# Optimization experiments

Hardware: AMD Instinct MI355X
Metric: run time of the kernel (lower is better)

The kernel has to match this reference:

```python
import jax, jax.numpy as jnp
import numpy as np

N = 50000
E = 800000
C_IN = 64
C_OUT = 64
K = 3  # Chebyshev order (num_stacks)
LAMBDA_MAX = 2.0


def setup_inputs() -> dict:
    key = jax.random.key(0)
    ks = jax.random.split(key, 32)
    inp = {
        'X': jax.random.normal(ks[0], (N, C_IN), dtype=jnp.float32),
        'edge_index': jax.random.randint(ks[1], (2, E), 0, N, dtype=jnp.int64),
        'edge_weight': jax.random.uniform(ks[2], (E,), dtype=jnp.float32),
        'H': jax.random.normal(ks[3], (N, C_OUT), dtype=jnp.float32),
        'C': jax.random.normal(ks[4], (N, C_OUT), dtype=jnp.float32),
    }
    # 8 ChebConvs: conv_{x,h}_{i,f,c,o}; x-convs map C_IN->C_OUT, h-convs C_OUT->C_OUT
    names_x = ['Wxi', 'Wxf', 'Wxc', 'Wxo']
    names_h = ['Whi', 'Whf', 'Whc', 'Who']
    i = 5
    for nx, nh in zip(names_x, names_h):
        inp[nx] = jax.random.normal(ks[i], (K, C_IN, C_OUT), dtype=jnp.float32) * (1.0 / np.sqrt(K * C_IN)); i += 1
        inp['b' + nx[1:]] = jax.random.normal(ks[i], (C_OUT,), dtype=jnp.float32) * 0.01; i += 1
        inp[nh] = jax.random.normal(ks[i], (K, C_OUT, C_OUT), dtype=jnp.float32) * (1.0 / np.sqrt(K * C_OUT)); i += 1
        inp['b' + nh[1:]] = jax.random.normal(ks[i], (C_OUT,), dtype=jnp.float32) * 0.01; i += 1
    # per-gate biases b_i, b_f, b_c, b_o of shape [1, C_OUT] (zero-initialized in torch)
    for nm in ['bi', 'bf', 'bc', 'bo']:
        inp[nm] = jax.random.normal(ks[i], (1, C_OUT), dtype=jnp.float32) * 0.01; i += 1
    return inp


def _cheb_norm(edge_index, edge_weight, n):
    # symmetric normalization: D^-1/2 W D^-1/2 (PyG get_laplacian 'sym')
    row, col = edge_index[0], edge_index[1]
    deg = jax.ops.segment_sum(edge_weight, row, num_segments=n)
    dinv = jnp.where(deg > 0, jax.lax.rsqrt(jnp.where(deg > 0, deg, 1.0)), 0.0)
    return dinv[row] * edge_weight * dinv[col]


def _cheb_conv(x, W, b, row, col, nw, n):
    # ChebConv: out = sum_k T_k(L_hat) x @ W[k] + b, with
    # L_hat v = (2/lambda_max) * (v - A_norm v) - v
    def Lhat(v):
        agg = jax.ops.segment_sum(nw[:, None] * v[col], row, num_segments=n)
        return (2.0 / LAMBDA_MAX) * (v - agg) - v
    Tx_prev = x
    out = x @ W[0]
    k = W.shape[0]
    if k > 1:
        Tx = Lhat(x)
        out = out + Tx @ W[1]
        for j in range(2, k):
            Tx_new = 2.0 * Lhat(Tx) - Tx_prev
            out = out + Tx_new @ W[j]
            Tx_prev, Tx = Tx, Tx_new
    return out + b


def reference(X, edge_index, edge_weight, H, C,
              Wxi, bxi, Whi, bhi, Wxf, bxf, Whf, bhf,
              Wxc, bxc, Whc, bhc, Wxo, bxo, Who, bho,
              bi, bf, bc, bo):
    n = X.shape[0]
    row, col = edge_index[0], edge_index[1]
    nw = _cheb_norm(edge_index, edge_weight, n)
    cc = lambda v, W, b: _cheb_conv(v, W, b, row, col, nw, n)
    I = jax.nn.sigmoid(cc(X, Wxi, bxi) + cc(H, Whi, bhi) + bi)
    F = jax.nn.sigmoid(cc(X, Wxf, bxf) + cc(H, Whf, bhf) + bf)
    T = jnp.tanh(cc(X, Wxc, bxc) + cc(H, Whc, bhc) + bc)
    C_new = F * C + I * T
    O = jax.nn.sigmoid(cc(X, Wxo, bxo) + cc(H, Who, bho) + bo)
    H_new = O * jnp.tanh(C_new)
    return (H_new, C_new)
```

## Files before the change

kernel.cpp:

```cpp
#include <hip/hip_runtime.h>

#define N_NODES 50000
#define N_PAD   50048
#define N_EDGES 800000
#define NBE4    782
#define NB_IL2  1563
#define NBKT    196
#define BCAP    4992

typedef __attribute__((ext_vector_type(8))) short bf16x8;
typedef __attribute__((ext_vector_type(4))) float f32x4;

__device__ __forceinline__ unsigned short f2bf(float f) {
    unsigned u = __float_as_uint(f);
    u = (u + 0x7fffu + ((u >> 16) & 1u)) >> 16;
    return (unsigned short)u;
}

__device__ __forceinline__ float fsig(float x) {
    x = fminf(fmaxf(x, -30.f), 30.f);
    float t = __expf(x);
    return __fdividef(t, 1.f + t);
}
__device__ __forceinline__ float ftanh(float x) {
    x = fminf(fmaxf(x, -15.f), 15.f);
    float t = __expf(2.f * x);
    return 1.f - __fdividef(2.f, t + 1.f);
}


__global__ __launch_bounds__(256) void k_prep(
    const void* __restrict__ eiraw,
    unsigned* __restrict__ hist,
    const float* __restrict__ X, const float* __restrict__ H, unsigned short* __restrict__ XH,
    const float* __restrict__ Wxi, const float* __restrict__ Whi,
    const float* __restrict__ Wxf, const float* __restrict__ Whf,
    const float* __restrict__ Wxc, const float* __restrict__ Whc,
    const float* __restrict__ Wxo, const float* __restrict__ Who,
    const float* __restrict__ bxi, const float* __restrict__ bhi,
    const float* __restrict__ bxf, const float* __restrict__ bhf,
    const float* __restrict__ bxc, const float* __restrict__ bhc,
    const float* __restrict__ bxo, const float* __restrict__ bho,
    const float* __restrict__ bgi, const float* __restrict__ bgf,
    const float* __restrict__ bgc, const float* __restrict__ bgo,
    unsigned short* __restrict__ Wf, float* __restrict__ ball) {
    __shared__ int sflag;
    __shared__ unsigned cnt[NBKT];
    int b = blockIdx.x, t = threadIdx.x;
    if (b < NBE4) {
        if (t == 0) sflag = 0;
        if (t < NBKT) cnt[t] = 0;
        __syncthreads();
        int si = b * 1024 + t;
        int sv = ((const int*)eiraw)[1 + 2 * si];
        if (sv) atomicOr(&sflag, 1);
        __syncthreads();
        int is32 = sflag;
#pragma unroll
        for (int k = 0; k < 4; k++) {
            int e = b * 1024 + k * 256 + t;
            if (e < N_EDGES) {
                int r = is32 ? ((const int*)eiraw)[e] : (int)(((const long long*)eiraw)[e]);
                atomicAdd(&cnt[r >> 8], 1u);
            }
        }
        __syncthreads();
        if (t < NBKT) hist[(size_t)t * NBE4 + b] = cnt[t];
        return;
    }
    int bb = b - NBE4;
    if (bb < NB_IL2) {
        int tt = bb * 256 + t;
        int node = tt >> 3, g = tt & 7;
        if (node >= N_NODES) return;
        const float* base = (g < 4) ? (X + (size_t)node * 64 + g * 16)
                                    : (H + (size_t)node * 64 + (g - 4) * 16);
        float4 v0 = ((const float4*)base)[0];
        float4 v1 = ((const float4*)base)[1];
        float4 v2 = ((const float4*)base)[2];
        float4 v3 = ((const float4*)base)[3];
        uint4 o0, o1;
        o0.x = (unsigned)f2bf(v0.x) | ((unsigned)f2bf(v0.y) << 16);
        o0.y = (unsigned)f2bf(v0.z) | ((unsigned)f2bf(v0.w) << 16);
        o0.z = (unsigned)f2bf(v1.x) | ((unsigned)f2bf(v1.y) << 16);
        o0.w = (unsigned)f2bf(v1.z) | ((unsigned)f2bf(v1.w) << 16);
        o1.x = (unsigned)f2bf(v2.x) | ((unsigned)f2bf(v2.y) << 16);
        o1.y = (unsigned)f2bf(v2.z) | ((unsigned)f2bf(v2.w) << 16);
        o1.z = (unsigned)f2bf(v3.x) | ((unsigned)f2bf(v3.y) << 16);
        o1.w = (unsigned)f2bf(v3.z) | ((unsigned)f2bf(v3.w) << 16);
        unsigned short* dst = XH + (size_t)node * 128 + g * 16;
        *(uint4*)dst = o0;
        *(uint4*)(dst + 8) = o1;
        return;
    }
    bb -= NB_IL2;
    if (bb < 48) {
        int flat = bb * 256 + t;
        int l = flat & 63, nt = (flat >> 6) & 15, ks = flat >> 10;
        int n = nt * 16 + (l & 15);
        int g = n >> 6, c = n & 63;
        const float* WX = (g == 0) ? Wxi : (g == 1) ? Wxf : (g == 2) ? Wxc : Wxo;
        const float* WH = (g == 0) ? Whi : (g == 1) ? Whf : (g == 2) ? Whc : Who;
        int k0 = ks * 32 + (l >> 4) * 8;
        unsigned short ov[8];
#pragma unroll
        for (int j = 0; j < 8; j++) {
            int k = k0 + j;
            int bsel = k >> 7, ch = k & 127;
            const float* W = (ch < 64) ? WX : WH;
            int kk = ch & 63;
            float v;
            if (bsel == 0)      v = W[kk * 64 + c] - W[2 * 4096 + kk * 64 + c];
            else if (bsel == 1) v = -W[4096 + kk * 64 + c];
            else                v = 2.f * W[2 * 4096 + kk * 64 + c];
            ov[j] = f2bf(v);
        }
        uint4 o;
        o.x = (unsigned)ov[0] | ((unsigned)ov[1] << 16);
        o.y = (unsigned)ov[2] | ((unsigned)ov[3] << 16);
        o.z = (unsigned)ov[4] | ((unsigned)ov[5] << 16);
        o.w = (unsigned)ov[6] | ((unsigned)ov[7] << 16);
        *(uint4*)(Wf + (size_t)flat * 8) = o;
    } else {
        int g = t >> 6, c = t & 63;
        const float* BX = (g == 0) ? bxi : (g == 1) ? bxf : (g == 2) ? bxc : bxo;
        const float* BH = (g == 0) ? bhi : (g == 1) ? bhf : (g == 2) ? bhc : bho;
        const float* BG = (g == 0) ? bgi : (g == 1) ? bgf : (g == 2) ? bgc : bgo;
        ball[t] = BX[c] + BH[c] + BG[c];
    }
}


__global__ __launch_bounds__(256) void k_bscan(unsigned* __restrict__ hist, unsigned* __restrict__ btot) {
    __shared__ unsigned s[256];
    int j = blockIdx.x, t = threadIdx.x;
    unsigned* row = hist + (size_t)j * NBE4;
    unsigned v[4];
#pragma unroll
    for (int k = 0; k < 4; k++) {
        int i = t * 4 + k;
        v[k] = (i < NBE4) ? row[i] : 0u;
    }
    unsigned tsum = v[0] + v[1] + v[2] + v[3];
    s[t] = tsum; __syncthreads();
    for (int d = 1; d < 256; d <<= 1) {
        unsigned a = (t >= d) ? s[t - d] : 0u;
        __syncthreads();
        s[t] += a;
        __syncthreads();
    }
    unsigned run = s[t] - tsum;
#pragma unroll
    for (int k = 0; k < 4; k++) {
        int i = t * 4 + k;
        if (i < NBE4) { unsigned c = v[k]; row[i] = run; run += c; }
    }
    if (t == 255) btot[j] = s[255];
}


__global__ __launch_bounds__(256) void k_btot(const unsigned* __restrict__ btot,
                                              unsigned* __restrict__ bbase, int* __restrict__ rp) {
    __shared__ unsigned s[256];
    int t = threadIdx.x;
    unsigned v = (t < NBKT) ? btot[t] : 0u;
    s[t] = v; __syncthreads();
    for (int d = 1; d < 256; d <<= 1) {
        unsigned a = (t >= d) ? s[t - d] : 0u;
        __syncthreads();
        s[t] += a;
        __syncthreads();
    }
    if (t < NBKT) bbase[t] = s[t] - v;
    if (t == 0) { bbase[NBKT] = N_EDGES; rp[N_NODES] = N_EDGES; }
}


__global__ __launch_bounds__(256) void k_scat(const void* __restrict__ eiraw, const float* __restrict__ w,
                                              const unsigned* __restrict__ hist, const unsigned* __restrict__ bbase,
                                              unsigned long long* __restrict__ ebuf) {
    __shared__ int sflag;
    __shared__ unsigned boff[NBKT];
    __shared__ unsigned cur[NBKT];
    int b = blockIdx.x, t = threadIdx.x;
    if (t == 0) sflag = 0;
    if (t < NBKT) { boff[t] = bbase[t] + hist[(size_t)t * NBE4 + b]; cur[t] = 0u; }
    __syncthreads();
    int si = b * 1024 + t;
    int sv = ((const int*)eiraw)[1 + 2 * si];
    if (sv) atomicOr(&sflag, 1);
    __syncthreads();
    int is32 = sflag;
#pragma unroll
    for (int k = 0; k < 4; k++) {
        int e = b * 1024 + k * 256 + t;
        if (e < N_EDGES) {
            int r, c;
            if (is32) { r = ((const int*)eiraw)[e]; c = ((const int*)eiraw)[N_EDGES + e]; }
            else      { r = (int)(((const long long*)eiraw)[e]); c = (int)(((const long long*)eiraw)[N_EDGES + e]); }
            float wv = w[e];
            int bk = r >> 8;
            unsigned lr = atomicAdd(&cur[bk], 1u);
            unsigned pos = boff[bk] + lr;
            ebuf[pos] = ((unsigned long long)(unsigned)r << 48)
                      | (((unsigned long long)(unsigned)c & 0xffffull) << 32)
                      | (unsigned long long)__float_as_uint(wv);
        }
    }
}


__global__ __launch_bounds__(1024) void k_build(const unsigned long long* __restrict__ ebuf,
                                                const unsigned* __restrict__ bbase,
                                                int* __restrict__ rp, float* __restrict__ dinv,
                                                int* __restrict__ colp, float* __restrict__ wraw) {
    __shared__ unsigned long long se[BCAP];
    __shared__ unsigned cnt[256];
    __shared__ float wsum[256];
    __shared__ unsigned off[256];
    __shared__ unsigned cur[256];
    int b = blockIdx.x, t = threadIdx.x;
    unsigned base = bbase[b], end = bbase[b + 1];
    int n = (int)(end - base);
    if (t < 256) { cnt[t] = 0u; wsum[t] = 0.f; }
    __syncthreads();
    for (int i = t; i < n; i += 1024) {
        unsigned long long e = ebuf[base + i];
        if (i < BCAP) se[i] = e;
        unsigned lr = (unsigned)(e >> 48) & 255u;
        atomicAdd(&cnt[lr], 1u);
        atomicAdd(&wsum[lr], __uint_as_float((unsigned)(e & 0xffffffffu)));
    }
    __syncthreads();
    if (t < 256) off[t] = cnt[t];
    __syncthreads();
    for (int d = 1; d < 256; d <<= 1) {
        unsigned a = 0u;
        if (t < 256 && t >= d) a = off[t - d];
        __syncthreads();
        if (t < 256) off[t] += a;
        __syncthreads();
    }
    if (t < 256) {
        unsigned excl = off[t] - cnt[t];
        off[t] = excl;
        cur[t] = excl;
        int row = b * 256 + t;
        if (row < N_NODES) {
            rp[row] = (int)(base + excl);
            float dg = wsum[t];
            dinv[row] = (dg > 0.f) ? rsqrtf(dg) : 0.f;
        }
    }
    __syncthreads();
    for (int i = t; i < n; i += 1024) {
        unsigned long long e = (i < BCAP) ? se[i] : ebuf[base + i];
        unsigned lr = (unsigned)(e >> 48) & 255u;
        unsigned p = atomicAdd(&cur[lr], 1u);
        int row = b * 256 + (int)lr;
        int c = (int)((e >> 32) & 0xffffu);
        colp[base + p] = (row << 16) | c;
        wraw[base + p] = __uint_as_float((unsigned)(e & 0xffffffffu));
    }
}


__global__ __launch_bounds__(256) void k_nw(const int* __restrict__ colp, const float* __restrict__ wraw,
                                            const float* __restrict__ dinv, float* __restrict__ nwp) {
    int e = blockIdx.x * 256 + threadIdx.x;
    if (e >= N_EDGES) return;
    unsigned rc = (unsigned)colp[e];
    nwp[e] = dinv[rc >> 16] * wraw[e] * dinv[rc & 0xffffu];
}


__global__ __launch_bounds__(256) void k_spmv_bf(const unsigned short* __restrict__ src,
                                                 unsigned short* __restrict__ dst,
                                                 const int* __restrict__ rp,
                                                 const int* __restrict__ colp, const float* __restrict__ nwp) {
    int wid = threadIdx.x >> 6, lane = threadIdx.x & 63;
    int node = blockIdx.x * 4 + wid;
    if (node >= N_NODES) return;
    int s = rp[node], e = rp[node + 1];
    float a0 = 0.f, a1 = 0.f;
    for (int jb = s; jb < e; jb += 8) {
        int   c[8]; float wv[8]; unsigned vv[8];
#pragma unroll
        for (int k = 0; k < 8; k++) {
            int j = jb + k;
            int jc = (j < e) ? j : (e - 1);
            c[k]  = colp[jc] & 0xffff;
            wv[k] = (j < e) ? nwp[jc] : 0.f;
        }
#pragma unroll
        for (int k = 0; k < 8; k++)
            vv[k] = *(const unsigned*)(src + (size_t)c[k] * 128 + lane * 2);
#pragma unroll
        for (int k = 0; k < 8; k++) {
            a0 = fmaf(wv[k], __uint_as_float(vv[k] << 16), a0);
            a1 = fmaf(wv[k], __uint_as_float(vv[k] & 0xffff0000u), a1);
        }
    }
    unsigned o = (unsigned)f2bf(a0) | ((unsigned)f2bf(a1) << 16);
    *(unsigned*)(dst + (size_t)node * 128 + lane * 2) = o;
}


__global__ __launch_bounds__(256) void k_gemm_mfma(
    const unsigned short* __restrict__ XH, const unsigned short* __restrict__ U1,
    const unsigned short* __restrict__ U2, const unsigned short* __restrict__ Wf,
    const float* __restrict__ ball, const float* __restrict__ C, float* __restrict__ out) {
    __shared__ __align__(16) uint4 Bs[2][1024];

    int t = threadIdx.x;
    int wid = t >> 6, lane = t & 63;
    int col = lane & 15, quad = lane >> 4;
    int m0 = blockIdx.x * 64 + wid * 16;
    int arow = m0 + col;

    f32x4 acc[16];
#pragma unroll
    for (int i = 0; i < 16; i++) acc[i] = (f32x4){0.f, 0.f, 0.f, 0.f};

    const unsigned short* srcs[3] = {XH, U1, U2};

    bf16x8 a_cur = *(const bf16x8*)(srcs[0] + (size_t)arow * 128 + quad * 8);
    const uint4* g0 = (const uint4*)Wf;
    uint4 p0 = g0[t], p1 = g0[t + 256], p2 = g0[t + 512], p3 = g0[t + 768];

    for (int ks = 0; ks < 12; ks++) {
        uint4* dstb = Bs[ks & 1];
        dstb[t] = p0; dstb[t + 256] = p1; dstb[t + 512] = p2; dstb[t + 768] = p3;
        __syncthreads();
        bf16x8 a_nxt = a_cur;
        if (ks < 11) {
            int ks1 = ks + 1;
            const uint4* g = (const uint4*)(Wf + (size_t)ks1 * 8192);
            p0 = g[t]; p1 = g[t + 256]; p2 = g[t + 512]; p3 = g[t + 768];
            a_nxt = *(const bf16x8*)(srcs[ks1 >> 2] + (size_t)arow * 128 + (ks1 & 3) * 32 + quad * 8);
        }
        const unsigned short* B = (const unsigned short*)Bs[ks & 1];
#pragma unroll
        for (int nt = 0; nt < 16; nt++) {
            bf16x8 bfrag = *(const bf16x8*)(B + nt * 512 + lane * 8);
            acc[nt] = __builtin_amdgcn_mfma_f32_16x16x32_bf16(a_cur, bfrag, acc[nt], 0, 0, 0);
        }
        a_cur = a_nxt;
    }

    float bI[4], bF[4], bT[4], bO[4];
#pragma unroll
    for (int cq = 0; cq < 4; cq++) {
        int c = cq * 16 + col;
        bI[cq] = ball[c]; bF[cq] = ball[64 + c]; bT[cq] = ball[128 + c]; bO[cq] = ball[192 + c];
    }
#pragma unroll
    for (int r = 0; r < 4; r++) {
        int node = m0 + quad * 4 + r;
        if (node >= N_NODES) continue;
#pragma unroll
        for (int cq = 0; cq < 4; cq++) {
            int c = cq * 16 + col;
            float ig = fsig(acc[0 + cq][r]  + bI[cq]);
            float fg = fsig(acc[4 + cq][r]  + bF[cq]);
            float tg = ftanh(acc[8 + cq][r] + bT[cq]);
            float og = fsig(acc[12 + cq][r] + bO[cq]);
            float cv = fmaf(fg, C[(size_t)node * 64 + c], ig * tg);
            out[(size_t)node * 64 + c] = og * ftanh(cv);
            out[(size_t)N_NODES * 64 + (size_t)node * 64 + c] = cv;
        }
    }
}


extern "C" void kernel_launch(void* const* d_in, const int* in_sizes, int n_in,
                              void* d_out, int out_size, void* d_ws, size_t ws_size,
                              hipStream_t stream) {
    const float* X   = (const float*)d_in[0];
    const void*  ei  = d_in[1];
    const float* w   = (const float*)d_in[2];
    const float* H   = (const float*)d_in[3];
    const float* C   = (const float*)d_in[4];
    const float* Wxi = (const float*)d_in[5];  const float* bxi = (const float*)d_in[6];
    const float* Whi = (const float*)d_in[7];  const float* bhi = (const float*)d_in[8];
    const float* Wxf = (const float*)d_in[9];  const float* bxf = (const float*)d_in[10];
    const float* Whf = (const float*)d_in[11]; const float* bhf = (const float*)d_in[12];
    const float* Wxc = (const float*)d_in[13]; const float* bxc = (const float*)d_in[14];
    const float* Whc = (const float*)d_in[15]; const float* bhc = (const float*)d_in[16];
    const float* Wxo = (const float*)d_in[17]; const float* bxo = (const float*)d_in[18];
    const float* Who = (const float*)d_in[19]; const float* bho = (const float*)d_in[20];
    const float* bgi = (const float*)d_in[21]; const float* bgf = (const float*)d_in[22];
    const float* bgc = (const float*)d_in[23]; const float* bgo = (const float*)d_in[24];
    float* out = (float*)d_out;

    char* ws = (char*)d_ws;
    size_t off = 0;
    auto alloc = [&](size_t bytes) -> char* {
        char* p = ws + off;
        off = (off + bytes + 255) & ~(size_t)255;
        return p;
    };
    unsigned* hist  = (unsigned*)alloc((size_t)NBKT * NBE4 * 4);
    unsigned* btot  = (unsigned*)alloc((NBKT + 1) * 4);
    unsigned* bbase = (unsigned*)alloc((NBKT + 1) * 4);
    unsigned long long* ebuf = (unsigned long long*)alloc((size_t)N_EDGES * 8);
    int*   rp   = (int*)alloc((N_NODES + 1) * 4);
    float* dinv = (float*)alloc(N_NODES * 4);
    int*   colp = (int*)alloc((size_t)(N_EDGES + 8) * 4);
    float* wraw = (float*)alloc((size_t)(N_EDGES + 8) * 4);
    float* nwp  = (float*)alloc((size_t)(N_EDGES + 8) * 4);
    unsigned short* XH = (unsigned short*)alloc((size_t)N_PAD * 128 * 2);
    unsigned short* U1 = (unsigned short*)alloc((size_t)N_PAD * 128 * 2);
    unsigned short* U2 = (unsigned short*)alloc((size_t)N_PAD * 128 * 2);
    unsigned short* Wf = (unsigned short*)alloc((size_t)12 * 16 * 64 * 8 * 2);
    float* ball = (float*)alloc(256 * 4);
    (void)ws_size; (void)in_sizes; (void)n_in; (void)out_size;

    k_prep<<<NBE4 + NB_IL2 + 49, 256, 0, stream>>>(ei, hist, X, H, XH,
                                                   Wxi, Whi, Wxf, Whf, Wxc, Whc, Wxo, Who,
                                                   bxi, bhi, bxf, bhf, bxc, bhc, bxo, bho,
                                                   bgi, bgf, bgc, bgo, Wf, ball);
    k_bscan<<<NBKT, 256, 0, stream>>>(hist, btot);
    k_btot<<<1, 256, 0, stream>>>(btot, bbase, rp);
    k_scat<<<NBE4, 256, 0, stream>>>(ei, w, hist, bbase, ebuf);
    k_build<<<NBKT, 1024, 0, stream>>>(ebuf, bbase, rp, dinv, colp, wraw);
    k_nw<<<(N_EDGES + 255) / 256, 256, 0, stream>>>(colp, wraw, dinv, nwp);
    k_spmv_bf<<<(N_NODES + 3) / 4, 256, 0, stream>>>(XH, U1, rp, colp, nwp);
    k_spmv_bf<<<(N_NODES + 3) / 4, 256, 0, stream>>>(U1, U2, rp, colp, nwp);
    k_gemm_mfma<<<(N_NODES + 63) / 64, 256, 0, stream>>>(XH, U1, U2, Wf, ball, C, out);
}
```

Measured before the change: 267.6 us.

## Split SpMV into column chunks and fold bucket-base scan into consumers

```diff
diff --git a/kernel.cpp b/kernel.cpp
--- a/kernel.cpp
+++ b/kernel.cpp
@@ -7,6 +7,7 @@
 #define NB_IL2  1563
 #define NBKT    196
 #define BCAP    4992
+#define NCHUNK  4
 
 typedef __attribute__((ext_vector_type(8))) short bf16x8;
 typedef __attribute__((ext_vector_type(4))) float f32x4;
@@ -159,32 +160,24 @@
 }
 
 
-__global__ __launch_bounds__(256) void k_btot(const unsigned* __restrict__ btot,
-                                              unsigned* __restrict__ bbase, int* __restrict__ rp) {
-    __shared__ unsigned s[256];
-    int t = threadIdx.x;
-    unsigned v = (t < NBKT) ? btot[t] : 0u;
-    s[t] = v; __syncthreads();
-    for (int d = 1; d < 256; d <<= 1) {
-        unsigned a = (t >= d) ? s[t - d] : 0u;
-        __syncthreads();
-        s[t] += a;
-        __syncthreads();
-    }
-    if (t < NBKT) bbase[t] = s[t] - v;
-    if (t == 0) { bbase[NBKT] = N_EDGES; rp[N_NODES] = N_EDGES; }
-}
-
-
 __global__ __launch_bounds__(256) void k_scat(const void* __restrict__ eiraw, const float* __restrict__ w,
-                                              const unsigned* __restrict__ hist, const unsigned* __restrict__ bbase,
+                                              const unsigned* __restrict__ hist, const unsigned* __restrict__ btot,
                                               unsigned long long* __restrict__ ebuf) {
     __shared__ int sflag;
+    __shared__ unsigned ssc[256];
     __shared__ unsigned boff[NBKT];
     __shared__ unsigned cur[NBKT];
     int b = blockIdx.x, t = threadIdx.x;
+    unsigned v = (t < NBKT) ? btot[t] : 0u;
+    ssc[t] = v; __syncthreads();
+    for (int d = 1; d < 256; d <<= 1) {
+        unsigned a = (t >= d) ? ssc[t - d] : 0u;
+        __syncthreads();
+        ssc[t] += a;
+        __syncthreads();
+    }
+    if (t < NBKT) { boff[t] = (ssc[t] - v) + hist[(size_t)t * NBE4 + b]; cur[t] = 0u; }
     if (t == 0) sflag = 0;
-    if (t < NBKT) { boff[t] = bbase[t] + hist[(size_t)t * NBE4 + b]; cur[t] = 0u; }
     __syncthreads();
     int si = b * 1024 + t;
     int sv = ((const int*)eiraw)[1 + 2 * si];
@@ -211,17 +204,29 @@
 
 
 __global__ __launch_bounds__(1024) void k_build(const unsigned long long* __restrict__ ebuf,
-                                                const unsigned* __restrict__ bbase,
+                                                const unsigned* __restrict__ btot,
                                                 int* __restrict__ rp, float* __restrict__ dinv,
                                                 int* __restrict__ colp, float* __restrict__ wraw) {
     __shared__ unsigned long long se[BCAP];
+    __shared__ unsigned ssc[256];
     __shared__ unsigned cnt[256];
     __shared__ float wsum[256];
     __shared__ unsigned off[256];
     __shared__ unsigned cur[256];
     int b = blockIdx.x, t = threadIdx.x;
-    unsigned base = bbase[b], end = bbase[b + 1];
+    if (t < 256) ssc[t] = (t < NBKT) ? btot[t] : 0u;
+    __syncthreads();
+    for (int d = 1; d < 256; d <<= 1) {
+        unsigned a = 0u;
+        if (t < 256 && t >= d) a = ssc[t - d];
+        __syncthreads();
+        if (t < 256) ssc[t] += a;
+        __syncthreads();
+    }
+    unsigned base = (b > 0) ? ssc[b - 1] : 0u;
+    unsigned end  = ssc[b];
     int n = (int)(end - base);
+    if (b == 0 && t == 0) rp[N_NODES] = N_EDGES;
     if (t < 256) { cnt[t] = 0u; wsum[t] = 0.f; }
     __syncthreads();
     for (int i = t; i < n; i += 1024) {
@@ -274,13 +279,15 @@
 }
 
 
-__global__ __launch_bounds__(256) void k_spmv_bf(const unsigned short* __restrict__ src,
+__global__ __launch_bounds__(256) void k_spmv_ch(const unsigned short* __restrict__ src,
                                                  unsigned short* __restrict__ dst,
                                                  const int* __restrict__ rp,
-                                                 const int* __restrict__ colp, const float* __restrict__ nwp) {
-    int wid = threadIdx.x >> 6, lane = threadIdx.x & 63;
-    int node = blockIdx.x * 4 + wid;
-    if (node >= N_NODES) return;
+                                                 const int* __restrict__ colp, const float* __restrict__ nwp,
+                                                 int ch) {
+    int t = threadIdx.x;
+    int node = blockIdx.x * 16 + (t >> 4);
+    int ls = t & 15;
+    int cofs = ch * 32;
     int s = rp[node], e = rp[node + 1];
     float a0 = 0.f, a1 = 0.f;
     for (int jb = s; jb < e; jb += 8) {
@@ -294,7 +301,7 @@
         }
 #pragma unroll
         for (int k = 0; k < 8; k++)
-            vv[k] = *(const unsigned*)(src + (size_t)c[k] * 128 + lane * 2);
+            vv[k] = *(const unsigned*)(src + (size_t)c[k] * 128 + cofs + ls * 2);
 #pragma unroll
         for (int k = 0; k < 8; k++) {
             a0 = fmaf(wv[k], __uint_as_float(vv[k] << 16), a0);
@@ -302,7 +309,7 @@
         }
     }
     unsigned o = (unsigned)f2bf(a0) | ((unsigned)f2bf(a1) << 16);
-    *(unsigned*)(dst + (size_t)node * 128 + lane * 2) = o;
+    *(unsigned*)(dst + (size_t)node * 128 + cofs + ls * 2) = o;
 }
 
 
@@ -402,7 +409,6 @@
     };
     unsigned* hist  = (unsigned*)alloc((size_t)NBKT * NBE4 * 4);
     unsigned* btot  = (unsigned*)alloc((NBKT + 1) * 4);
-    unsigned* bbase = (unsigned*)alloc((NBKT + 1) * 4);
     unsigned long long* ebuf = (unsigned long long*)alloc((size_t)N_EDGES * 8);
     int*   rp   = (int*)alloc((N_NODES + 1) * 4);
     float* dinv = (float*)alloc(N_NODES * 4);
@@ -421,11 +427,12 @@
                                                    bxi, bhi, bxf, bhf, bxc, bhc, bxo, bho,
                                                    bgi, bgf, bgc, bgo, Wf, ball);
     k_bscan<<<NBKT, 256, 0, stream>>>(hist, btot);
-    k_btot<<<1, 256, 0, stream>>>(btot, bbase, rp);
-    k_scat<<<NBE4, 256, 0, stream>>>(ei, w, hist, bbase, ebuf);
-    k_build<<<NBKT, 1024, 0, stream>>>(ebuf, bbase, rp, dinv, colp, wraw);
+    k_scat<<<NBE4, 256, 0, stream>>>(ei, w, hist, btot, ebuf);
+    k_build<<<NBKT, 1024, 0, stream>>>(ebuf, btot, rp, dinv, colp, wraw);
     k_nw<<<(N_EDGES + 255) / 256, 256, 0, stream>>>(colp, wraw, dinv, nwp);
-    k_spmv_bf<<<(N_NODES + 3) / 4, 256, 0, stream>>>(XH, U1, rp, colp, nwp);
-    k_spmv_bf<<<(N_NODES + 3) / 4, 256, 0, stream>>>(U1, U2, rp, colp, nwp);
+    for (int ch = 0; ch < NCHUNK; ch++) {
+        k_spmv_ch<<<N_NODES / 16, 256, 0, stream>>>(XH, U1, rp, colp, nwp, ch);
+        k_spmv_ch<<<N_NODES / 16, 256, 0, stream>>>(U1, U2, rp, colp, nwp, ch);
+    }
     k_gemm_mfma<<<(N_NODES + 63) / 64, 256, 0, stream>>>(XH, U1, U2, Wf, ball, C, out);
 }
```

Measured after the change: 320.0 us. 1.2x slower.
